# Kernel tuning notes

Hardware: AMD Instinct MI355X
Metric: run time of the kernel (lower is better)

## Reference

```python
import jax, jax.numpy as jnp
import numpy as np

NUM_DIHEDRALS = 3
# Idealized backbone geometry (picometers / radians), as in RGN/pNeRF.
BOND_LENGTHS = np.array([145.801, 152.326, 132.868], dtype=np.float32)  # N-CA, CA-C, C-N
BOND_ANGLES = np.array([2.124, 1.941, 2.028], dtype=np.float32)


def setup_inputs() -> dict:
    key = jax.random.key(0)
    num_steps, batch = 2048, 512
    flat_dihedrals = jax.random.uniform(
        key, (num_steps * batch, NUM_DIHEDRALS),
        minval=-np.pi, maxval=np.pi, dtype=jnp.float32)
    return {"flat_dihedrals": flat_dihedrals, "batch_size": batch}


def _l2_normalize(v, eps=1e-12):
    return v / jnp.sqrt(jnp.sum(v * v, axis=-1, keepdims=True) + eps)


def dihedral_to_point(dihedral):
    # dihedral: [L, B, 3] -> points in local frames: [3L, B, 3]
    r_cos_theta = np.float32(BOND_LENGTHS * np.cos(np.pi - BOND_ANGLES))  # [3]
    r_sin_theta = np.float32(BOND_LENGTHS * np.sin(np.pi - BOND_ANGLES))  # [3]
    L, B, _ = dihedral.shape
    pt_x = jnp.broadcast_to(jnp.asarray(r_cos_theta), (L, B, NUM_DIHEDRALS))
    pt_y = jnp.cos(dihedral) * r_sin_theta
    pt_z = jnp.sin(dihedral) * r_sin_theta
    point = jnp.stack([pt_x, pt_y, pt_z], axis=-1)      # [L, B, 3, 3]
    return point.reshape(L * NUM_DIHEDRALS, B, 3)       # [3L, B, 3]


def point_to_coordinate(points):
    # points: [N, B, 3]; sequential NeRF rigid-body chain extension.
    B = points.shape[1]
    init = np.array([[-np.sqrt(0.5), np.sqrt(1.5), 0.0],
                     [-np.sqrt(2.0), 0.0, 0.0],
                     [0.0, 0.0, 0.0]], dtype=np.float32)
    a = jnp.broadcast_to(jnp.asarray(init[0]), (B, 3))
    b = jnp.broadcast_to(jnp.asarray(init[1]), (B, 3))
    c = jnp.broadcast_to(jnp.asarray(init[2]), (B, 3))

    def step(carry, p):
        a, b, c = carry
        bc = _l2_normalize(c - b)                      # [B, 3]
        n = _l2_normalize(jnp.cross(b - a, bc))        # [B, 3]
        # Rotation matrix with columns [bc, n x bc, n]
        m = jnp.stack([bc, jnp.cross(n, bc), n], axis=-1)   # [B, 3, 3]
        coord = jnp.einsum('bij,bj->bi', m, p) + c          # [B, 3]
        return (b, c, coord), coord

    _, coords = jax.lax.scan(step, (a, b, c), points)
    return coords  # [N, B, 3]


def reference(flat_dihedrals, batch_size):
    num_steps = flat_dihedrals.shape[0] // batch_size
    dihedrals = flat_dihedrals.reshape(num_steps, batch_size, NUM_DIHEDRALS)
    points = dihedral_to_point(dihedrals)
    coordinates = point_to_coordinate(points)
    return coordinates
```

## Files before the change

### kernel.cpp

```cpp
#include <hip/hip_runtime.h>
#include <math.h>

#define BATCH 512
#define FRAGS 256
#define GROUP 16
#define NGRP  (FRAGS/GROUP)
#define BTILE 32
#define NTILE (BATCH/BTILE)
#define RPF   8
#define READY 0x5EADBEEF

__device__ __forceinline__ void compose(const float* A, const float* B, float* D) {
    float d[12];
    #pragma unroll
    for (int i = 0; i < 3; ++i) {
        #pragma unroll
        for (int j = 0; j < 3; ++j)
            d[i*3+j] = A[i*3+0]*B[0*3+j] + A[i*3+1]*B[1*3+j] + A[i*3+2]*B[2*3+j];
        d[9+i] = A[i*3+0]*B[9] + A[i*3+1]*B[10] + A[i*3+2]*B[11] + A[9+i];
    }
    #pragma unroll
    for (int k = 0; k < 12; ++k) D[k] = d[k];
}

__device__ __forceinline__ void frame_of(
    float ax, float ay, float az,
    float bx, float by, float bz,
    float cx, float cy, float cz,
    float* out )
{
    float bcx = cx - bx, bcy = cy - by, bcz = cz - bz;
    float inv = rsqrtf(bcx*bcx + bcy*bcy + bcz*bcz + 1e-12f);
    bcx *= inv; bcy *= inv; bcz *= inv;
    float bax = bx - ax, bay = by - ay, baz = bz - az;
    float nx = bay*bcz - baz*bcy;
    float ny = baz*bcx - bax*bcz;
    float nz = bax*bcy - bay*bcx;
    inv = rsqrtf(nx*nx + ny*ny + nz*nz + 1e-12f);
    nx *= inv; ny *= inv; nz *= inv;
    float mx = ny*bcz - nz*bcy;
    float my = nz*bcx - nx*bcz;
    float mz = nx*bcy - ny*bcx;
    out[0] = bcx; out[1] = mx; out[2] = nx;
    out[3] = bcy; out[4] = my; out[5] = ny;
    out[6] = bcz; out[7] = mz; out[8] = nz;
    out[9] = cx; out[10] = cy; out[11] = cz;
}

__device__ __forceinline__ void nerf_step(
    float ax, float ay, float az,
    float bx, float by, float bz,
    float cx, float cy, float cz,
    float px, float py, float pz,
    float& ox, float& oy, float& oz)
{
    float bcx = cx - bx, bcy = cy - by, bcz = cz - bz;
    float inv = rsqrtf(bcx*bcx + bcy*bcy + bcz*bcz + 1e-12f);
    bcx *= inv; bcy *= inv; bcz *= inv;
    float bax = bx - ax, bay = by - ay, baz = bz - az;
    float nx = bay*bcz - baz*bcy;
    float ny = baz*bcx - bax*bcz;
    float nz = bax*bcy - bay*bcx;
    inv = rsqrtf(nx*nx + ny*ny + nz*nz + 1e-12f);
    nx *= inv; ny *= inv; nz *= inv;
    float mx = ny*bcz - nz*bcy;
    float my = nz*bcx - nx*bcz;
    float mz = nx*bcy - ny*bcx;
    ox = bcx*px + mx*py + nx*pz + cx;
    oy = bcy*px + my*py + ny*pz + cy;
    oz = bcz*px + mz*py + nz*pz + cz;
}

__device__ __forceinline__ void lane_consts(int b, float* rcl, float* rsl) {
    const float PI = 3.14159265358979323846f;
    float rc[3], rs[3];
    rc[0] = 145.801f * cosf(PI - 2.124f); rs[0] = 145.801f * sinf(PI - 2.124f);
    rc[1] = 152.326f * cosf(PI - 1.941f); rs[1] = 152.326f * sinf(PI - 1.941f);
    rc[2] = 132.868f * cosf(PI - 2.028f); rs[2] = 132.868f * sinf(PI - 2.028f);
    const int d0 = b % 3, d1 = (b + 2) % 3, d2 = (b + 1) % 3;
    rcl[0] = rc[d0]; rcl[1] = rc[d1]; rcl[2] = rc[d2];
    rsl[0] = rs[d0]; rsl[1] = rs[d1]; rsl[2] = rs[d2];
}

__global__ void __launch_bounds__(GROUP * BTILE) coord_onepass(
    const float* __restrict__ dih, float* __restrict__ T,
    int* __restrict__ flags, float* __restrict__ out)
{
    const int btile = blockIdx.x & (NTILE - 1);
    const int g     = blockIdx.x >> 4;
    const int bsub  = threadIdx.x & (BTILE - 1);
    const int j     = threadIdx.x >> 5;
    const int f     = g * GROUP + j;
    const int b     = btile * BTILE + bsub;

    __shared__ float S[GROUP * BTILE * 13];
    __shared__ float Elds[BTILE * 13];
    float* Srow = &S[(size_t)threadIdx.x * 13];

    float rcl[3], rsl[3];
    lane_consts(b, rcl, rsl);

    const float IAX = -0.70710678118654752f, IAY = 1.22474487139158905f;
    const float IBX = -1.41421356237309505f;

    float ax = IAX, ay = IAY, az = 0.0f;
    float bx = IBX, by = 0.0f, bz = 0.0f;
    float cx = 0.0f, cy = 0.0f, cz = 0.0f;

    #pragma unroll 1
    for (int r = 0; r < RPF; ++r) {
        const float* src = dih + (size_t)(f * RPF + r) * (3 * BATCH) + b;
        float d0 = src[0];
        float d1 = src[BATCH];
        float d2 = src[2 * BATCH];
        float sn, cs, ox, oy, oz;
        __sincosf(d0, &sn, &cs);
        nerf_step(ax, ay, az, bx, by, bz, cx, cy, cz,
                  rcl[0], cs * rsl[0], sn * rsl[0], ox, oy, oz);
        ax = bx; ay = by; az = bz; bx = cx; by = cy; bz = cz;
        cx = ox; cy = oy; cz = oz;
        __sincosf(d1, &sn, &cs);
        nerf_step(ax, ay, az, bx, by, bz, cx, cy, cz,
                  rcl[1], cs * rsl[1], sn * rsl[1], ox, oy, oz);
        ax = bx; ay = by; az = bz; bx = cx; by = cy; bz = cz;
        cx = ox; cy = oy; cz = oz;
        __sincosf(d2, &sn, &cs);
        nerf_step(ax, ay, az, bx, by, bz, cx, cy, cz,
                  rcl[2], cs * rsl[2], sn * rsl[2], ox, oy, oz);
        ax = bx; ay = by; az = bz; bx = cx; by = cy; bz = cz;
        cx = ox; cy = oy; cz = oz;
    }

    {
        float h[12];
        frame_of(ax, ay, az, bx, by, bz, cx, cy, cz, h);
        #pragma unroll
        for (int k = 0; k < 12; ++k) Srow[k] = h[k];
    }
    __syncthreads();

    float tmp[12];
    #pragma unroll 1
    for (int o = 1; o < GROUP; o <<= 1) {
        const bool act = (j >= o);
        if (act) compose(&S[(size_t)(threadIdx.x - o * BTILE) * 13], Srow, tmp);
        __syncthreads();
        if (act) {
            #pragma unroll
            for (int k = 0; k < 12; ++k) Srow[k] = tmp[k];
        }
        __syncthreads();
    }

    if (j == GROUP - 1) {
        #pragma unroll
        for (int k = 0; k < 12; ++k)
            __hip_atomic_store(&T[((size_t)g * 12 + k) * BATCH + b], Srow[k],
                               __ATOMIC_RELAXED, __HIP_MEMORY_SCOPE_AGENT);
    }
    __syncthreads();
    if (threadIdx.x == 0)
        __hip_atomic_store(&flags[g * NTILE + btile], READY,
                           __ATOMIC_RELEASE, __HIP_MEMORY_SCOPE_AGENT);

    float G[12];
    if (g > 0) {
        if ((int)threadIdx.x < g) {
            while (__hip_atomic_load(&flags[threadIdx.x * NTILE + btile],
                                     __ATOMIC_RELAXED, __HIP_MEMORY_SCOPE_AGENT)
                   != READY) {
                __builtin_amdgcn_s_sleep(1);
            }
        }
        if (j == 0) {
            __builtin_amdgcn_fence(__ATOMIC_ACQUIRE, "agent");
            float E[12];
            #pragma unroll
            for (int k = 0; k < 12; ++k)
                E[k] = __hip_atomic_load(&T[(size_t)k * BATCH + b],
                                         __ATOMIC_RELAXED, __HIP_MEMORY_SCOPE_AGENT);
            #pragma unroll 1
            for (int gp = 1; gp < g; ++gp) {
                float tg[12];
                #pragma unroll
                for (int k = 0; k < 12; ++k)
                    tg[k] = __hip_atomic_load(&T[((size_t)gp * 12 + k) * BATCH + b],
                                              __ATOMIC_RELAXED, __HIP_MEMORY_SCOPE_AGENT);
                compose(E, tg, E);
            }
            #pragma unroll
            for (int k = 0; k < 12; ++k) Elds[bsub * 13 + k] = E[k];
        }
        __syncthreads();
        #pragma unroll
        for (int k = 0; k < 12; ++k) G[k] = Elds[bsub * 13 + k];
    } else {
        G[0]=1.f; G[1]=0.f; G[2]=0.f;
        G[3]=0.f; G[4]=1.f; G[5]=0.f;
        G[6]=0.f; G[7]=0.f; G[8]=1.f;
        G[9]=0.f; G[10]=0.f; G[11]=0.f;
    }
    if (j > 0) {
        compose(G, &S[(size_t)(threadIdx.x - BTILE) * 13], G);
    }

    ax = G[0]*IAX + G[1]*IAY + G[9];
    ay = G[3]*IAX + G[4]*IAY + G[10];
    az = G[6]*IAX + G[7]*IAY + G[11];
    bx = G[0]*IBX + G[9];
    by = G[3]*IBX + G[10];
    bz = G[6]*IBX + G[11];
    cx = G[9]; cy = G[10]; cz = G[11];

    #pragma unroll 1
    for (int r = 0; r < RPF; ++r) {
        const float* src = dih + (size_t)(f * RPF + r) * (3 * BATCH) + b;
        float d0 = src[0];
        float d1 = src[BATCH];
        float d2 = src[2 * BATCH];
        float* dst = out + (((size_t)f * (3 * RPF) + r * 3) * BATCH + b) * 3;
        float sn, cs, ox, oy, oz;

        __sincosf(d0, &sn, &cs);
        nerf_step(ax, ay, az, bx, by, bz, cx, cy, cz,
                  rcl[0], cs * rsl[0], sn * rsl[0], ox, oy, oz);
        ax = bx; ay = by; az = bz; bx = cx; by = cy; bz = cz;
        cx = ox; cy = oy; cz = oz;
        dst[0] = ox; dst[1] = oy; dst[2] = oz;

        __sincosf(d1, &sn, &cs);
        nerf_step(ax, ay, az, bx, by, bz, cx, cy, cz,
                  rcl[1], cs * rsl[1], sn * rsl[1], ox, oy, oz);
        ax = bx; ay = by; az = bz; bx = cx; by = cy; bz = cz;
        cx = ox; cy = oy; cz = oz;
        dst += 3 * BATCH;
        dst[0] = ox; dst[1] = oy; dst[2] = oz;

        __sincosf(d2, &sn, &cs);
        nerf_step(ax, ay, az, bx, by, bz, cx, cy, cz,
                  rcl[2], cs * rsl[2], sn * rsl[2], ox, oy, oz);
        ax = bx; ay = by; az = bz; bx = cx; by = cy; bz = cz;
        cx = ox; cy = oy; cz = oz;
        dst += 3 * BATCH;
        dst[0] = ox; dst[1] = oy; dst[2] = oz;
    }
}

extern "C" void kernel_launch(void* const* d_in, const int* in_sizes, int n_in,
                              void* d_out, int out_size, void* d_ws, size_t ws_size,
                              hipStream_t stream) {
    const float* dih = (const float*)d_in[0];
    float* out = (float*)d_out;
    float* T = (float*)d_ws;
    int* flags = (int*)(T + (size_t)NGRP * 12 * BATCH);

    coord_onepass<<<dim3(NGRP * NTILE), dim3(GROUP * BTILE), 0, stream>>>(
        dih, T, flags, out);
    (void)ws_size; (void)n_in; (void)out_size; (void)in_sizes;
}
```

Before: 97.63 us.

## Split single-pass decoupled scan into two kernels, dropping spin-wait flags

```diff
diff --git a/kernel.cpp b/kernel.cpp
--- a/kernel.cpp
+++ b/kernel.cpp
@@ -8,7 +8,6 @@
 #define BTILE 32
 #define NTILE (BATCH/BTILE)
 #define RPF   8
-#define READY 0x5EADBEEF
 
 __device__ __forceinline__ void compose(const float* A, const float* B, float* D) {
     float d[12];
@@ -82,9 +81,9 @@
     rsl[0] = rs[d0]; rsl[1] = rs[d1]; rsl[2] = rs[d2];
 }
 
-__global__ void __launch_bounds__(GROUP * BTILE) coord_onepass(
-    const float* __restrict__ dih, float* __restrict__ T,
-    int* __restrict__ flags, float* __restrict__ out)
+
+__global__ void __launch_bounds__(GROUP * BTILE) frames_kernel(
+    const float* __restrict__ dih, float* __restrict__ P)
 {
     const int btile = blockIdx.x & (NTILE - 1);
     const int g     = blockIdx.x >> 4;
@@ -94,41 +93,33 @@
     const int b     = btile * BTILE + bsub;
 
     __shared__ float S[GROUP * BTILE * 13];
-    __shared__ float Elds[BTILE * 13];
     float* Srow = &S[(size_t)threadIdx.x * 13];
 
     float rcl[3], rsl[3];
     lane_consts(b, rcl, rsl);
 
-    const float IAX = -0.70710678118654752f, IAY = 1.22474487139158905f;
-    const float IBX = -1.41421356237309505f;
-
-    float ax = IAX, ay = IAY, az = 0.0f;
-    float bx = IBX, by = 0.0f, bz = 0.0f;
+    float ax = -0.70710678118654752f, ay = 1.22474487139158905f, az = 0.0f;
+    float bx = -1.41421356237309505f, by = 0.0f, bz = 0.0f;
     float cx = 0.0f, cy = 0.0f, cz = 0.0f;
 
-    #pragma unroll 1
+    #pragma unroll
     for (int r = 0; r < RPF; ++r) {
         const float* src = dih + (size_t)(f * RPF + r) * (3 * BATCH) + b;
-        float d0 = src[0];
-        float d1 = src[BATCH];
-        float d2 = src[2 * BATCH];
-        float sn, cs, ox, oy, oz;
-        __sincosf(d0, &sn, &cs);
-        nerf_step(ax, ay, az, bx, by, bz, cx, cy, cz,
-                  rcl[0], cs * rsl[0], sn * rsl[0], ox, oy, oz);
-        ax = bx; ay = by; az = bz; bx = cx; by = cy; bz = cz;
-        cx = ox; cy = oy; cz = oz;
-        __sincosf(d1, &sn, &cs);
-        nerf_step(ax, ay, az, bx, by, bz, cx, cy, cz,
-                  rcl[1], cs * rsl[1], sn * rsl[1], ox, oy, oz);
-        ax = bx; ay = by; az = bz; bx = cx; by = cy; bz = cz;
-        cx = ox; cy = oy; cz = oz;
-        __sincosf(d2, &sn, &cs);
-        nerf_step(ax, ay, az, bx, by, bz, cx, cy, cz,
-                  rcl[2], cs * rsl[2], sn * rsl[2], ox, oy, oz);
-        ax = bx; ay = by; az = bz; bx = cx; by = cy; bz = cz;
-        cx = ox; cy = oy; cz = oz;
+        float dd[3];
+        dd[0] = src[0];
+        dd[1] = src[BATCH];
+        dd[2] = src[2 * BATCH];
+        #pragma unroll
+        for (int k = 0; k < 3; ++k) {
+            float sn, cs;
+            __sincosf(dd[k], &sn, &cs);
+            float ox, oy, oz;
+            nerf_step(ax, ay, az, bx, by, bz, cx, cy, cz,
+                      rcl[k], cs * rsl[k], sn * rsl[k], ox, oy, oz);
+            ax = bx; ay = by; az = bz;
+            bx = cx; by = cy; bz = cz;
+            cx = ox; cy = oy; cz = oz;
+        }
     }
 
     {
@@ -140,7 +131,7 @@
     __syncthreads();
 
     float tmp[12];
-    #pragma unroll 1
+    #pragma unroll
     for (int o = 1; o < GROUP; o <<= 1) {
         const bool act = (j >= o);
         if (act) compose(&S[(size_t)(threadIdx.x - o * BTILE) * 13], Srow, tmp);
@@ -152,40 +143,43 @@
         __syncthreads();
     }
 
-    if (j == GROUP - 1) {
-        #pragma unroll
-        for (int k = 0; k < 12; ++k)
-            __hip_atomic_store(&T[((size_t)g * 12 + k) * BATCH + b], Srow[k],
-                               __ATOMIC_RELAXED, __HIP_MEMORY_SCOPE_AGENT);
-    }
-    __syncthreads();
-    if (threadIdx.x == 0)
-        __hip_atomic_store(&flags[g * NTILE + btile], READY,
-                           __ATOMIC_RELEASE, __HIP_MEMORY_SCOPE_AGENT);
+    float* dst = P + ((size_t)f * BATCH + b) * 12;
+    #pragma unroll
+    for (int k = 0; k < 12; ++k) dst[k] = Srow[k];
+}
+
+__global__ void __launch_bounds__(GROUP * BTILE) emit_kernel(
+    const float* __restrict__ dih, const float* __restrict__ P,
+    float* __restrict__ out)
+{
+    const int btile = blockIdx.x & (NTILE - 1);
+    const int g     = blockIdx.x >> 4;
+    const int bsub  = threadIdx.x & (BTILE - 1);
+    const int j     = threadIdx.x >> 5;
+    const int f     = g * GROUP + j;
+    const int b     = btile * BTILE + bsub;
+
+    __shared__ float Elds[BTILE * 13];
+
+    float rcl[3], rsl[3];
+    lane_consts(b, rcl, rsl);
+
+    const float IAX = -0.70710678118654752f, IAY = 1.22474487139158905f;
+    const float IBX = -1.41421356237309505f;
 
     float G[12];
     if (g > 0) {
-        if ((int)threadIdx.x < g) {
-            while (__hip_atomic_load(&flags[threadIdx.x * NTILE + btile],
-                                     __ATOMIC_RELAXED, __HIP_MEMORY_SCOPE_AGENT)
-                   != READY) {
-                __builtin_amdgcn_s_sleep(1);
-            }
-        }
         if (j == 0) {
-            __builtin_amdgcn_fence(__ATOMIC_ACQUIRE, "agent");
             float E[12];
+            const float* s0 = P + ((size_t)(GROUP - 1) * BATCH + b) * 12;
             #pragma unroll
-            for (int k = 0; k < 12; ++k)
-                E[k] = __hip_atomic_load(&T[(size_t)k * BATCH + b],
-                                         __ATOMIC_RELAXED, __HIP_MEMORY_SCOPE_AGENT);
+            for (int k = 0; k < 12; ++k) E[k] = s0[k];
             #pragma unroll 1
             for (int gp = 1; gp < g; ++gp) {
+                const float* sg = P + ((size_t)(gp * GROUP + GROUP - 1) * BATCH + b) * 12;
                 float tg[12];
                 #pragma unroll
-                for (int k = 0; k < 12; ++k)
-                    tg[k] = __hip_atomic_load(&T[((size_t)gp * 12 + k) * BATCH + b],
-                                              __ATOMIC_RELAXED, __HIP_MEMORY_SCOPE_AGENT);
+                for (int k = 0; k < 12; ++k) tg[k] = sg[k];
                 compose(E, tg, E);
             }
             #pragma unroll
@@ -201,16 +195,20 @@
         G[9]=0.f; G[10]=0.f; G[11]=0.f;
     }
     if (j > 0) {
-        compose(G, &S[(size_t)(threadIdx.x - BTILE) * 13], G);
-    }
-
-    ax = G[0]*IAX + G[1]*IAY + G[9];
-    ay = G[3]*IAX + G[4]*IAY + G[10];
-    az = G[6]*IAX + G[7]*IAY + G[11];
-    bx = G[0]*IBX + G[9];
-    by = G[3]*IBX + G[10];
-    bz = G[6]*IBX + G[11];
-    cx = G[9]; cy = G[10]; cz = G[11];
+        const float* sp = P + ((size_t)(f - 1) * BATCH + b) * 12;
+        float pp[12];
+        #pragma unroll
+        for (int k = 0; k < 12; ++k) pp[k] = sp[k];
+        compose(G, pp, G);
+    }
+
+    float ax = G[0]*IAX + G[1]*IAY + G[9];
+    float ay = G[3]*IAX + G[4]*IAY + G[10];
+    float az = G[6]*IAX + G[7]*IAY + G[11];
+    float bx = G[0]*IBX + G[9];
+    float by = G[3]*IBX + G[10];
+    float bz = G[6]*IBX + G[11];
+    float cx = G[9], cy = G[10], cz = G[11];
 
     #pragma unroll 1
     for (int r = 0; r < RPF; ++r) {
@@ -251,10 +249,9 @@
                               hipStream_t stream) {
     const float* dih = (const float*)d_in[0];
     float* out = (float*)d_out;
-    float* T = (float*)d_ws;
-    int* flags = (int*)(T + (size_t)NGRP * 12 * BATCH);
-
-    coord_onepass<<<dim3(NGRP * NTILE), dim3(GROUP * BTILE), 0, stream>>>(
-        dih, T, flags, out);
+    float* P = (float*)d_ws;
+
+    frames_kernel<<<dim3(NGRP * NTILE), dim3(GROUP * BTILE), 0, stream>>>(dih, P);
+    emit_kernel<<<dim3(NGRP * NTILE), dim3(GROUP * BTILE), 0, stream>>>(dih, P, out);
     (void)ws_size; (void)n_in; (void)out_size; (void)in_sizes;
 }
```

Result: faster. 93.47 us (-4.3%).
